# Kernel tuning notes

Hardware: AMD Instinct MI355X
Metric: run time of the kernel (lower is better)

## Reference

```python
import jax, jax.numpy as jnp
import numpy as np
from jax import lax

K = 47          # SH coefficient count
HID = 96        # cascade hidden channels
S = 300         # sampling directions
NC = 4          # number of cascades
IDX = np.r_[0:16, 45:47]  # low-order SH indices used by c_init


def _conv(x, w, bias):
    # x: (B, C, D, H, W); w: (O, I, kd, kh, kw)
    y = lax.conv_general_dilated(x, w, (1, 1, 1), 'VALID',
                                 dimension_numbers=('NCDHW', 'OIDHW', 'NCDHW'))
    return y + bias[None, :, None, None, None]


def _cascade(c, w1, b1, w2, b2, w3, b3):
    # c: (B, D, H, W, 47, 1) -> (B, D-2, H-2, W-2, 94, 1)
    x = jnp.transpose(c[..., 0], (0, 4, 1, 2, 3))       # (B,47,D,H,W)
    x = jax.nn.relu(_conv(x, w1, b1))                    # valid 3x3x3 -> spatial-2
    x = jax.nn.relu(_conv(x, w2, b2))                    # 1x1x1
    x = _conv(x, w3, b3)                                 # 1x1x1 -> 94 channels
    return jnp.transpose(x, (0, 2, 3, 4, 1))[..., None]


def _bsolve(A, rhs):
    # A: (B,K,K) identical across voxels; rhs: (B,D,H,W,K,1)
    # Factor once per batch, apply to all voxel RHS vectors at once.
    B, D, H, W, Kk, _ = rhs.shape
    r = rhs[..., 0].reshape(B, D * H * W, Kk).swapaxes(1, 2)  # (B,K,N)
    x = jnp.linalg.solve(A, r)
    return x.swapaxes(1, 2).reshape(B, D, H, W, Kk, 1)


def _gate(cc):
    return cc[..., :K, :] * jax.nn.sigmoid(cc[..., K:, :])


def setup_inputs() -> dict:
    key = jax.random.key(0)
    ks = jax.random.split(key, 8)
    B, D, H, W = 1, 48, 48, 48
    sc = 0.05
    inp = {
        'b': jax.random.normal(ks[0], (B, D, H, W, S, 1), jnp.float32),
        'AQ': jax.random.normal(ks[1], (B, S, K), jnp.float32) * 0.1,
        'w1': jax.random.normal(ks[2], (NC, HID, K, 3, 3, 3), jnp.float32) * sc,
        'b1': jnp.zeros((NC, HID), jnp.float32),
        'w2': jax.random.normal(ks[3], (NC, HID, HID, 1, 1, 1), jnp.float32) * sc,
        'b2': jnp.zeros((NC, HID), jnp.float32),
        'w3': jax.random.normal(ks[4], (NC, 2 * K, HID, 1, 1, 1), jnp.float32) * sc,
        'b3': jnp.zeros((NC, 2 * K), jnp.float32),
        'deep_reg': jnp.float32(0.05),
    }
    return inp


def reference(b, AQ, w1, b1, w2, b2, w3, b3, deep_reg):
    # AQ^T b per voxel: (B,D,H,W,47,1); AQ^T AQ once per batch: (B,47,47)
    AQ_Tb = jnp.einsum('bnk,bdhwn->bdhwk', AQ, b[..., 0])[..., None]
    AQ_TAQ = jnp.einsum('bnk,bnl->bkl', AQ, AQ)

    # --- c_init: low-order (18-coef) regularized least squares ---
    AQs = AQ[:, :, IDX]                                   # (B,300,18)
    A18 = jnp.einsum('bnk,bnl->bkl', AQs, AQs) + 0.01 * jnp.eye(18, dtype=AQ.dtype)
    c_hat = _bsolve(A18, AQ_Tb[..., IDX, :])
    c = jnp.zeros(b.shape[:4] + (K, 1), b.dtype)
    c = c.at[..., :16, :].set(c_hat[..., :16, :])
    c = c.at[..., 45:, :].set(c_hat[..., 16:, :])

    # --- cascades + data consistency ---
    A = AQ_TAQ + deep_reg * jnp.eye(K, dtype=AQ.dtype)
    for i in range(NC):
        cc = _cascade(c, w1[i], b1[i], w2[i], b2[i], w3[i], b3[i])
        if i == 0:
            g = _gate(cc)
        else:
            g = c[:, 1:-1, 1:-1, 1:-1] + _gate(cc)       # residual connection
        n = i + 1
        c = _bsolve(A, AQ_Tb[:, n:-n, n:-n, n:-n] + deep_reg * g)
    return c
```

## Files before the change

kernel.cpp:

```cpp
#include <hip/hip_runtime.h>
#include <math.h>

#define NS 300
#define NK 47
#define NHID 96
#define NFULL 48

typedef __attribute__((ext_vector_type(8))) short bf16x8;
typedef __attribute__((ext_vector_type(4))) float f32x4;
typedef __attribute__((ext_vector_type(4))) short s16x4;

__device__ __forceinline__ float sigmoidf(float x){ return 1.0f/(1.0f+expf(-x)); }
__device__ __forceinline__ short f2bf(float f){
    union { float f; unsigned u; } v; v.f = f;
    unsigned r = v.u + 0x7fffu + ((v.u >> 16) & 1u);
    return (short)(r >> 16);
}
__device__ __forceinline__ float bf2f(short s){
    union { unsigned u; float f; } v; v.u = ((unsigned)(unsigned short)s) << 16;
    return v.f;
}
__device__ __forceinline__ unsigned pk(short lo, short hi){
    return (unsigned)(unsigned short)lo | ((unsigned)(unsigned short)hi << 16);
}


#define AQP 328
#define P47 72
#define P18 40
__global__ __launch_bounds__(256) void prep_small(const float* __restrict__ AQ,
                           const float* __restrict__ dreg_p,
                           float* __restrict__ Ainv18, short* __restrict__ Ainvbf,
                           short* __restrict__ Bseq){
    __shared__ __align__(16) char smem[93824];
    short* AQh = (short*)smem;
    short* AQl = AQh + 48*AQP;
    float* Gf  = (float*)(smem + 62976);
    short* M47 = (short*)smem;
    short* M18 = (short*)(smem + 72960);
    float* rs47 = (float*)(smem + 93440);
    float* rs18 = rs47 + 48;
    float* shc  = rs18 + 32;

    const int tid = threadIdx.x;
    const int lane = tid & 63;
    const int wv  = tid >> 6;
    const int l15 = lane & 15;
    const int lhi = lane >> 4;
    const float dreg = dreg_p[0];

    #pragma unroll 4
    for (int idx = tid; idx < 48*AQP; idx += 256){
        int k = idx / AQP, n = idx - k*AQP;
        float a = (k < 47 && n < 300) ? AQ[n*NK + k] : 0.f;
        short h = f2bf(a);
        short l = f2bf(a - bf2f(h));
        AQh[idx] = h; AQl[idx] = l;
        if (n < 320){
            int step = n >> 5, lh = (n >> 3) & 3, j = n & 7;
            int t = k >> 4, kl = k & 15;
            int base = ((step*3 + t)*2)*512 + (lh*16 + kl)*8 + j;
            Bseq[base]       = h;
            Bseq[base + 512] = l;
        }
    }
    __syncthreads();

    const int t0 = wv, t1 = wv + 4, t2 = wv + 8;
    f32x4 g0, g1, g2;
    {
        auto gram = [&](int t) -> f32x4 {
            int tt = (t < 9) ? t : t - 9;
            int k0 = (tt/3)*16, l0 = (tt%3)*16;
            f32x4 a = (f32x4){0.f,0.f,0.f,0.f};
            for (int ks = 0; ks < 10; ++ks){
                int off = ks*32 + lhi*8;
                bf16x8 ph = *(const bf16x8*)&AQh[(k0+l15)*AQP + off];
                bf16x8 pl = *(const bf16x8*)&AQl[(k0+l15)*AQP + off];
                bf16x8 qh = *(const bf16x8*)&AQh[(l0+l15)*AQP + off];
                bf16x8 ql = *(const bf16x8*)&AQl[(l0+l15)*AQP + off];
                a = __builtin_amdgcn_mfma_f32_16x16x32_bf16(ph, qh, a, 0,0,0);
                a = __builtin_amdgcn_mfma_f32_16x16x32_bf16(pl, qh, a, 0,0,0);
                a = __builtin_amdgcn_mfma_f32_16x16x32_bf16(ph, ql, a, 0,0,0);
            }
            return a;
        };
        g0 = gram(t0); g1 = gram(t1); g2 = gram(t2);
    }
    __syncthreads();

    for (int i = tid; i < 8*48*P47; i += 256) M47[i] = 0;
    for (int i = tid; i < 8*32*P18; i += 256) M18[i] = 0;
    {
        auto wrG = [&](int t, f32x4 a){
            if (t < 9){
                int k0 = (t/3)*16, l0 = (t%3)*16;
                #pragma unroll
                for (int r = 0; r < 4; ++r)
                    Gf[(k0 + lhi*4 + r)*52 + (l0 + l15)] = a[r];
            }
        };
        wrG(t0,g0); wrG(t1,g1); wrG(t2,g2);
    }
    __syncthreads();

    short* Ah  = M47;            short* Al  = M47 + 3456;
    short* Xah = M47 + 2*3456;   short* Xal = M47 + 3*3456;
    short* Xbh = M47 + 4*3456;   short* Xbl = M47 + 5*3456;
    short* Zh  = M47 + 6*3456;   short* Zl  = M47 + 7*3456;
    short* Bh8 = M18;            short* Bl8 = M18 + 1280;
    short* Xah8= M18 + 2*1280;   short* Xal8= M18 + 3*1280;
    short* Xbh8= M18 + 4*1280;   short* Xbl8= M18 + 5*1280;
    short* Zh8 = M18 + 6*1280;   short* Zl8 = M18 + 7*1280;

    {
        auto wrA = [&](int t, f32x4 a){
            if (t < 9){
                int k0 = (t/3)*16, l0 = (t%3)*16;
                #pragma unroll
                for (int r = 0; r < 4; ++r){
                    int k = k0 + lhi*4 + r, l = l0 + l15;
                    float v = (k < 47 && l < 47) ? a[r] + (k==l ? dreg : 0.f)
                                                 : ((k==l) ? 1.f : 0.f);
                    short h = f2bf(v);
                    Ah[k*P47 + l] = h;
                    Al[k*P47 + l] = f2bf(v - bf2f(h));
                }
            }
        };
        wrA(t0,g0); wrA(t1,g1); wrA(t2,g2);
    }
    if (tid < 48){
        float s = 1.f;
        if (tid < 47){
            s = dreg;
            for (int l = 0; l < 47; ++l) s += fabsf(Gf[tid*52 + l]);
        }
        rs47[tid] = s;
    }
    if (tid >= 64 && tid < 96){
        int r = tid - 64;
        float s = 1.f;
        if (r < 18){
            int gk = (r < 16) ? r : r + 29;
            s = 0.f;
            for (int l = 0; l < 18; ++l){
                int gl = (l < 16) ? l : l + 29;
                s += fabsf(Gf[gk*52 + gl] + ((l==r) ? 0.01f : 0.f));
            }
        }
        rs18[r] = s;
    }
    for (int e = tid; e < 32*32; e += 256){
        int k = e >> 5, l = e & 31;
        float v;
        if (k < 18 && l < 18){
            int gk = (k < 16) ? k : k + 29;
            int gl = (l < 16) ? l : l + 29;
            v = Gf[gk*52 + gl] + ((k==l) ? 0.01f : 0.f);
        } else v = (k==l) ? 1.f : 0.f;
        short h = f2bf(v);
        Bh8[k*P18 + l] = h;
        Bl8[k*P18 + l] = f2bf(v - bf2f(h));
    }
    __syncthreads();

    if (tid == 0){
        float m = 0.f;
        for (int i = 0; i < 48; ++i) m = fmaxf(m, rs47[i]);
        shc[0] = 1.f / m;
    }
    if (tid == 1){
        float m = 0.f;
        for (int i = 0; i < 32; ++i) m = fmaxf(m, rs18[i]);
        shc[1] = 1.f / m;
    }
    __syncthreads();

    if (tid < 48){
        float c = shc[0];
        short h = f2bf(c);
        Xah[tid*P47 + tid] = h;
        Xal[tid*P47 + tid] = f2bf(c - bf2f(h));
    } else if (tid >= 64 && tid < 96){
        int r = tid - 64;
        float c = shc[1];
        short h = f2bf(c);
        Xah8[r*P18 + r] = h;
        Xal8[r*P18 + r] = f2bf(c - bf2f(h));
    }
    __syncthreads();

    auto mmT = [&](int t, const short* Ph, const short* Pl,
                   const short* Qh, const short* Ql) -> f32x4 {
        int tt = (t < 9) ? t : t - 9;
        int k0 = (tt/3)*16, l0 = (tt%3)*16;
        f32x4 a = (f32x4){0.f,0.f,0.f,0.f};
        #pragma unroll
        for (int kk = 0; kk < 2; ++kk){
            int off = kk*32 + lhi*8;
            bf16x8 ph = *(const bf16x8*)&Ph[(k0+l15)*P47 + off];
            bf16x8 pl = *(const bf16x8*)&Pl[(k0+l15)*P47 + off];
            bf16x8 qh = *(const bf16x8*)&Qh[(l0+l15)*P47 + off];
            bf16x8 ql = *(const bf16x8*)&Ql[(l0+l15)*P47 + off];
            a = __builtin_amdgcn_mfma_f32_16x16x32_bf16(ph, qh, a, 0,0,0);
            a = __builtin_amdgcn_mfma_f32_16x16x32_bf16(pl, qh, a, 0,0,0);
            a = __builtin_amdgcn_mfma_f32_16x16x32_bf16(ph, ql, a, 0,0,0);
        }
        return a;
    };
    auto mm8 = [&](const short* Ph, const short* Pl,
                   const short* Qh, const short* Ql) -> f32x4 {
        int k0 = (wv >> 1)*16, l0 = (wv & 1)*16;
        int off = lhi*8;
        bf16x8 ph = *(const bf16x8*)&Ph[(k0+l15)*P18 + off];
        bf16x8 pl = *(const bf16x8*)&Pl[(k0+l15)*P18 + off];
        bf16x8 qh = *(const bf16x8*)&Qh[(l0+l15)*P18 + off];
        bf16x8 ql = *(const bf16x8*)&Ql[(l0+l15)*P18 + off];
        f32x4 a = (f32x4){0.f,0.f,0.f,0.f};
        a = __builtin_amdgcn_mfma_f32_16x16x32_bf16(ph, qh, a, 0,0,0);
        a = __builtin_amdgcn_mfma_f32_16x16x32_bf16(pl, qh, a, 0,0,0);
        a = __builtin_amdgcn_mfma_f32_16x16x32_bf16(ph, ql, a, 0,0,0);
        return a;
    };

    short *Xch = Xah, *Xcl = Xal, *Xnh = Xbh, *Xnl = Xbl;
    short *Xch8 = Xah8, *Xcl8 = Xal8, *Xnh8 = Xbh8, *Xnl8 = Xbl8;

    for (int it = 0; it < 10; ++it){
        f32x4 y0 = mmT(t0, Ah, Al, Xch, Xcl);
        f32x4 y1 = mmT(t1, Ah, Al, Xch, Xcl);
        f32x4 y2 = mmT(t2, Ah, Al, Xch, Xcl);
        f32x4 y8 = mm8(Bh8, Bl8, Xch8, Xcl8);
        auto wrZ = [&](int t, f32x4 a){
            if (t < 9){
                int k0 = (t/3)*16, l0 = (t%3)*16;
                #pragma unroll
                for (int r = 0; r < 4; ++r){
                    int k = k0 + lhi*4 + r, l = l0 + l15;
                    float z = ((k==l) ? 2.f : 0.f) - a[r];
                    short h = f2bf(z);
                    Zh[k*P47 + l] = h;
                    Zl[k*P47 + l] = f2bf(z - bf2f(h));
                }
            }
        };
        wrZ(t0,y0); wrZ(t1,y1); wrZ(t2,y2);
        {
            int k0 = (wv >> 1)*16, l0 = (wv & 1)*16;
            #pragma unroll
            for (int r = 0; r < 4; ++r){
                int k = k0 + lhi*4 + r, l = l0 + l15;
                float z = ((k==l) ? 2.f : 0.f) - y8[r];
                short h = f2bf(z);
                Zh8[k*P18 + l] = h;
                Zl8[k*P18 + l] = f2bf(z - bf2f(h));
            }
        }
        __syncthreads();
        f32x4 x0 = mmT(t0, Xch, Xcl, Zh, Zl);
        f32x4 x1 = mmT(t1, Xch, Xcl, Zh, Zl);
        f32x4 x2 = mmT(t2, Xch, Xcl, Zh, Zl);
        f32x4 x8 = mm8(Xch8, Xcl8, Zh8, Zl8);
        if (it < 9){
            auto wrX = [&](int t, f32x4 a){
                if (t < 9){
                    int k0 = (t/3)*16, l0 = (t%3)*16;
                    #pragma unroll
                    for (int r = 0; r < 4; ++r){
                        int k = k0 + lhi*4 + r, l = l0 + l15;
                        short h = f2bf(a[r]);
                        Xnh[k*P47 + l] = h;
                        Xnl[k*P47 + l] = f2bf(a[r] - bf2f(h));
                    }
                }
            };
            wrX(t0,x0); wrX(t1,x1); wrX(t2,x2);
            int k0 = (wv >> 1)*16, l0 = (wv & 1)*16;
            #pragma unroll
            for (int r = 0; r < 4; ++r){
                int k = k0 + lhi*4 + r, l = l0 + l15;
                short h = f2bf(x8[r]);
                Xnh8[k*P18 + l] = h;
                Xnl8[k*P18 + l] = f2bf(x8[r] - bf2f(h));
            }
        } else {
            auto wrF = [&](int t, f32x4 a){
                if (t < 9){
                    int k0 = (t/3)*16, l0 = (t%3)*16;
                    #pragma unroll
                    for (int r = 0; r < 4; ++r){
                        int k = k0 + lhi*4 + r, l = l0 + l15;
                        float v = (k < 47 && l < 47) ? a[r] : 0.f;
                        Ainvbf[k*64 + l] = f2bf(v);
                    }
                }
            };
            wrF(t0,x0); wrF(t1,x1); wrF(t2,x2);
            int k0 = (wv >> 1)*16, l0 = (wv & 1)*16;
            #pragma unroll
            for (int r = 0; r < 4; ++r){
                int k = k0 + lhi*4 + r, l = l0 + l15;
                if (k < 18 && l < 18) Ainv18[k*18 + l] = x8[r];
            }
        }
        __syncthreads();
        short* tp;
        tp = Xch; Xch = Xnh; Xnh = tp;
        tp = Xcl; Xcl = Xnl; Xnl = tp;
        tp = Xch8; Xch8 = Xnh8; Xnh8 = tp;
        tp = Xcl8; Xcl8 = Xnl8; Xnl8 = tp;
    }

    for (int e = tid; e < 48*16; e += 256){
        int k = e >> 4, j = e & 15;
        Ainvbf[k*64 + 48 + j] = 0;
    }
}

__global__ __launch_bounds__(256) void aqtb_mfma(const float* __restrict__ b,
                                                 const short* __restrict__ Bseq,
                                                 float* __restrict__ AQ_Tb){
    const int lane = threadIdx.x & 63;
    const int wv   = threadIdx.x >> 6;
    const int l15  = lane & 15;
    const int lhi  = lane >> 4;
    const int vrow = blockIdx.x*64 + wv*16 + l15;
    const float* brow = b + (size_t)vrow*NS;
    const short* bs = Bseq + lane*8;

    f32x4 acc[3];
    #pragma unroll
    for (int t = 0; t < 3; ++t) acc[t] = (f32x4){0.f,0.f,0.f,0.f};

    f32x4 q[3][2];
    #pragma unroll
    for (int s = 0; s < 3; ++s){
        const int n0 = s*32 + lhi*8;
        q[s][0] = *(const f32x4*)(brow + n0);
        q[s][1] = *(const f32x4*)(brow + n0 + 4);
    }

    #pragma unroll
    for (int step = 0; step < 10; ++step){
        float x[8];
        #pragma unroll
        for (int j = 0; j < 4; ++j){
            x[j]     = q[step%3][0][j];
            x[4 + j] = q[step%3][1][j];
        }
        if (step + 3 < 9){
            const int n0 = (step+3)*32 + lhi*8;
            q[step%3][0] = *(const f32x4*)(brow + n0);
            q[step%3][1] = *(const f32x4*)(brow + n0 + 4);
        } else if (step + 3 == 9){
            const int n0 = 288 + lhi*8;
            #pragma unroll
            for (int j = 0; j < 4; ++j){
                int n = n0 + j;
                q[step%3][0][j] = (n < NS) ? brow[n] : 0.f;
                int n2 = n0 + 4 + j;
                q[step%3][1][j] = (n2 < NS) ? brow[n2] : 0.f;
            }
        }
        bf16x8 Ah, Al;
        #pragma unroll
        for (int j = 0; j < 8; ++j){
            short h = f2bf(x[j]);
            Ah[j] = h;
            Al[j] = f2bf(x[j] - bf2f(h));
        }
        const short* bstep = bs + step*3072;
        #pragma unroll
        for (int t = 0; t < 3; ++t){
            bf16x8 Bh = *(const bf16x8*)(bstep + t*1024);
            bf16x8 Bl = *(const bf16x8*)(bstep + t*1024 + 512);
            acc[t] = __builtin_amdgcn_mfma_f32_16x16x32_bf16(Ah, Bh, acc[t], 0, 0, 0);
            acc[t] = __builtin_amdgcn_mfma_f32_16x16x32_bf16(Al, Bh, acc[t], 0, 0, 0);
            acc[t] = __builtin_amdgcn_mfma_f32_16x16x32_bf16(Ah, Bl, acc[t], 0, 0, 0);
        }
    }

    const int vbase = blockIdx.x*64 + wv*16 + lhi*4;
    #pragma unroll
    for (int t = 0; t < 3; ++t){
        int k = t*16 + l15;
        if (k < NK){
            #pragma unroll
            for (int r = 0; r < 4; ++r)
                AQ_Tb[(size_t)(vbase + r)*48 + k] = acc[t][r];
        }
    }
}

__global__ void conv_w1_bf16(const float* __restrict__ w1, short* __restrict__ wbf){
    int idx = blockIdx.x*256 + threadIdx.x;
    if (idx >= 4*27*96) return;
    int o = idx % 96; int rest = idx / 96; int s = rest % 27; int i = rest / 27;
    const float* src = w1 + ((size_t)i*96 + o)*1269 + s;
    short* dst = wbf + (size_t)idx*64;
    #pragma unroll
    for (int ci = 0; ci < 47; ++ci) dst[ci] = f2bf(src[ci*27]);
    #pragma unroll
    for (int ci = 47; ci < 64; ++ci) dst[ci] = 0;
}

__global__ void conv_w23_bf16(const float* __restrict__ w2, const float* __restrict__ w3,
                              short* __restrict__ w2bf, short* __restrict__ w3bf){
    int idx = blockIdx.x*256 + threadIdx.x;
    if (idx >= 768) return;
    if (idx < 384){
        const float* src = w2 + (size_t)idx*96;
        short* dst = w2bf + (size_t)idx*96;
        for (int k = 0; k < 96; ++k) dst[k] = f2bf(src[k]);
    } else {
        int j = idx - 384;
        int i = j / 96, o = j % 96;
        short* dst = w3bf + (size_t)j*96;
        if (o < 94){
            const float* src = w3 + ((size_t)i*94 + o)*96;
            for (int k = 0; k < 96; ++k) dst[k] = f2bf(src[k]);
        } else {
            for (int k = 0; k < 96; ++k) dst[k] = 0;
        }
    }
}

__global__ void init_c(const float* __restrict__ AQ_Tb, const float* __restrict__ Ainv18,
                       short* __restrict__ c64, int nvox){
    int v = blockIdx.x*blockDim.x + threadIdx.x;
    if (v >= nvox) return;
    float rhs[18];
    {
        const float* row = AQ_Tb + (size_t)v*48;
        f32x4 r0 = *(const f32x4*)(row + 0);
        f32x4 r1 = *(const f32x4*)(row + 4);
        f32x4 r2 = *(const f32x4*)(row + 8);
        f32x4 r3 = *(const f32x4*)(row + 12);
        #pragma unroll
        for (int j = 0; j < 4; ++j){
            rhs[j] = r0[j]; rhs[4+j] = r1[j]; rhs[8+j] = r2[j]; rhs[12+j] = r3[j];
        }
        rhs[16] = row[45];
        rhs[17] = row[46];
    }
    short row[64];
    #pragma unroll
    for (int k = 0; k < 64; ++k) row[k] = 0;
    #pragma unroll
    for (int r = 0; r < 18; ++r){
        float acc = 0.f;
        #pragma unroll
        for (int j = 0; j < 18; ++j) acc += Ainv18[r*18 + j] * rhs[j];
        row[(r < 16) ? r : 29 + r] = f2bf(acc);
    }
    int x = v % 48; int t2 = v / 48; int y = t2 % 48; int z = t2 / 48;
    short* base = c64 + (size_t)(z*48 + y)*3072;
    #pragma unroll
    for (int g = 0; g < 8; ++g)
        *(bf16x8*)(base + (size_t)(g*48 + x)*8) = *(const bf16x8*)&row[g*8];
}

__device__ __forceinline__ void stage_w(const short* __restrict__ src, short* dst, int tid){
    #pragma unroll
    for (int it = 0; it < 5; ++it){
        int d = (it*512 + tid) * 16;
        if (d < 36864){
            bf16x8 v = *(const bf16x8*)((const char*)src + d);
            int ds = d ^ (((d >> 7) & 7) << 4);
            *(bf16x8*)((char*)dst + ds) = v;
        }
    }
}

__global__ __launch_bounds__(512, 4) void conv1_mfma(const short* __restrict__ c64,
                                                     const short* __restrict__ wbf,
                                                     const float* __restrict__ b1,
                                                     short* __restrict__ h,
                                                     int Ni, int Mi){
    __shared__ short wlds[2][18432];
    const int tid = threadIdx.x;
    const int lane = tid & 63;
    const int wid  = tid >> 6;
    const int l15 = lane & 15;
    const int lhi = lane >> 4;
    const int z0 = blockIdx.z;
    const int x0 = blockIdx.x * 16;
    const int yw = blockIdx.y * 16 + wid * 2;

    f32x4 acc[2][6];
    #pragma unroll
    for (int yr = 0; yr < 2; ++yr)
        #pragma unroll
        for (int t = 0; t < 6; ++t) acc[yr][t] = (f32x4){0.f,0.f,0.f,0.f};

    stage_w(wbf, &wlds[0][0], tid);

    const int grpstride = Ni*8;
    for (int p = 0; p < 9; ++p){
        __syncthreads();
        if (p < 8) stage_w(wbf + (size_t)(p+1)*18432, &wlds[(p+1)&1][0], tid);
        const char* wb = (const char*)&wlds[p&1][0];
        const int dz = p / 3;
        const int dy = p - dz*3;
        const int gzN = (z0 + dz)*Ni;

        #pragma unroll
        for (int dx = 0; dx < 3; ++dx){
            int gx = min(x0 + l15 + dx, Ni-1);
            const short* arow[2];
            #pragma unroll
            for (int yr = 0; yr < 2; ++yr){
                int gy = min(yw + yr + dy, Ni-1);
                arow[yr] = c64 + (size_t)(gzN + gy)*Ni*64 + (size_t)lhi*grpstride + gx*8;
            }
            #pragma unroll
            for (int kk = 0; kk < 2; ++kk){
                bf16x8 a0 = *(const bf16x8*)(arow[0] + kk*4*grpstride);
                bf16x8 a1 = *(const bf16x8*)(arow[1] + kk*4*grpstride);
                #pragma unroll
                for (int t = 0; t < 6; ++t){
                    int d = ((dx*96 + t*16 + l15)*64 + kk*32 + lhi*8) * 2;
                    d ^= ((d >> 7) & 7) << 4;
                    bf16x8 b = *(const bf16x8*)(wb + d);
                    acc[0][t] = __builtin_amdgcn_mfma_f32_16x16x32_bf16(a0, b, acc[0][t], 0, 0, 0);
                    acc[1][t] = __builtin_amdgcn_mfma_f32_16x16x32_bf16(a1, b, acc[1][t], 0, 0, 0);
                }
            }
        }
    }

    #pragma unroll
    for (int yr = 0; yr < 2; ++yr){
        int yy = yw + yr;
        if (yy >= Mi) continue;
        #pragma unroll
        for (int t = 0; t < 6; ++t){
            int och = t*16 + l15;
            float bias = b1[och];
            #pragma unroll
            for (int r = 0; r < 4; ++r){
                int xx = x0 + lhi*4 + r;
                if (xx < Mi){
                    size_t vo = ((size_t)(z0*Mi + yy)*Mi + xx)*NHID + och;
                    h[vo] = f2bf(fmaxf(acc[yr][t][r] + bias, 0.f));
                }
            }
        }
    }
}

__global__ __launch_bounds__(256) void cascade_mfma(const short* __restrict__ h,
                                                    const short* __restrict__ cin64,
                                                    const float* __restrict__ AQ_Tb,
                                                    const short* __restrict__ w2bf,
                                                    const float* __restrict__ b2,
                                                    const short* __restrict__ w3bf,
                                                    const float* __restrict__ b3,
                                                    const short* __restrict__ Ainvbf,
                                                    const float* __restrict__ dreg_p,
                                                    short* __restrict__ c64out,
                                                    float* __restrict__ fout,
                                                    int Mi, int off, int iter, int final_i){
    __shared__ short bufA[64][112];
    __shared__ short bufB[64][112];
    const int tid = threadIdx.x;
    const int lane = tid & 63;
    const int wv  = tid >> 6;
    const int l15 = lane & 15;
    const int lhi = lane >> 4;
    const int nvox = Mi*Mi*Mi;
    const int v0 = blockIdx.x * 64;
    const float dreg = dreg_p[0];

    for (int f = tid; f < 64*24; f += 256){
        int v = f / 24, c = f % 24;
        int gv = v0 + v;
        s16x4 val = (s16x4){0,0,0,0};
        if (gv < nvox) val = *(const s16x4*)(h + (size_t)gv*NHID + c*4);
        *(s16x4*)&bufA[v][c*4] = val;
    }
    __syncthreads();

    const int vox = wv*16 + l15;

    {
        f32x4 acc2[6];
        #pragma unroll
        for (int m = 0; m < 6; ++m) acc2[m] = (f32x4){0.f,0.f,0.f,0.f};
        #pragma unroll
        for (int ks = 0; ks < 3; ++ks){
            bf16x8 bfr = *(const bf16x8*)&bufA[vox][lhi*8 + ks*32];
            #pragma unroll
            for (int m = 0; m < 6; ++m){
                bf16x8 a = *(const bf16x8*)(w2bf + (size_t)(m*16 + l15)*96 + lhi*8 + ks*32);
                acc2[m] = __builtin_amdgcn_mfma_f32_16x16x32_bf16(a, bfr, acc2[m], 0, 0, 0);
            }
        }
        #pragma unroll
        for (int m = 0; m < 6; ++m){
            int o0 = m*16 + lhi*4;
            float x0 = fmaxf(acc2[m][0] + b2[o0+0], 0.f);
            float x1 = fmaxf(acc2[m][1] + b2[o0+1], 0.f);
            float x2 = fmaxf(acc2[m][2] + b2[o0+2], 0.f);
            float x3 = fmaxf(acc2[m][3] + b2[o0+3], 0.f);
            *(unsigned*)&bufB[vox][o0]     = pk(f2bf(x0), f2bf(x1));
            *(unsigned*)&bufB[vox][o0 + 2] = pk(f2bf(x2), f2bf(x3));
        }
    }

    {
        f32x4 acc3[6];
        #pragma unroll
        for (int m = 0; m < 6; ++m) acc3[m] = (f32x4){0.f,0.f,0.f,0.f};
        #pragma unroll
        for (int ks = 0; ks < 3; ++ks){
            bf16x8 bfr = *(const bf16x8*)&bufB[vox][lhi*8 + ks*32];
            #pragma unroll
            for (int m = 0; m < 6; ++m){
                bf16x8 a = *(const bf16x8*)(w3bf + (size_t)(m*16 + l15)*96 + lhi*8 + ks*32);
                acc3[m] = __builtin_amdgcn_mfma_f32_16x16x32_bf16(a, bfr, acc3[m], 0, 0, 0);
            }
        }
        #pragma unroll
        for (int m = 0; m < 6; ++m){
            int o0 = m*16 + lhi*4;
            float xv[4];
            #pragma unroll
            for (int e = 0; e < 4; ++e){
                int o = o0 + e;
                xv[e] = (o < 94) ? acc3[m][e] + b3[o] : 0.f;
            }
            if (o0 + 3 < 47){
                *(unsigned*)&bufA[vox][o0]     = pk(f2bf(xv[0]), f2bf(xv[1]));
                *(unsigned*)&bufA[vox][o0 + 2] = pk(f2bf(xv[2]), f2bf(xv[3]));
            } else {
                #pragma unroll
                for (int e = 0; e < 4; ++e){
                    int o = o0 + e;
                    bufA[vox][o + (o >= 47)] = f2bf(xv[e]);
                }
            }
        }
    }
    __syncthreads();

    short (*rhsL)[64] = (short(*)[64])&bufB[0][0];
    {
        int v = tid >> 2, q = tid & 3;
        int gv = v0 + v;
        int z = 0, y = 0, x = 0;
        bool live = (gv < nvox);
        if (live){
            z = gv / (Mi*Mi);
            int r = gv % (Mi*Mi);
            y = r / Mi; x = r % Mi;
        }
        const int Nin = Mi + 2;
        const size_t rbase = (size_t)((z+1)*Nin + (y+1))*Nin*64;
        const float* aqr = AQ_Tb + ((size_t)((z+off)*NFULL + (y+off))*NFULL + (x+off))*48;

        auto do_group = [&](int g){
            const int k0 = g*8;
            bf16x8 cc1 = *(const bf16x8*)&bufA[v][k0];
            bf16x8 cc2 = *(const bf16x8*)&bufA[v][48 + k0];
            bf16x8 cv = (bf16x8){0,0,0,0,0,0,0,0};
            if (iter > 0)
                cv = *(const bf16x8*)&cin64[rbase + (size_t)(g*Nin + (x+1))*8];
            f32x4 aq0 = *(const f32x4*)(aqr + k0);
            f32x4 aq1 = *(const f32x4*)(aqr + k0 + 4);
            short outs[8];
            #pragma unroll
            for (int j = 0; j < 8; ++j){
                int k = k0 + j;
                if (live && k < 47){
                    float gt = bf2f(cc1[j]) * sigmoidf(bf2f(cc2[j]));
                    if (iter > 0) gt += bf2f(cv[j]);
                    float aq = (j < 4) ? aq0[j] : aq1[j-4];
                    outs[j] = f2bf(aq + dreg * gt);
                } else outs[j] = 0;
            }
            *(bf16x8*)&rhsL[v][k0] = *(const bf16x8*)outs;
        };
        do_group(q);
        if (q < 2){
            do_group(q + 4);
        } else {
            *(bf16x8*)&rhsL[v][48 + (q - 2)*8] = (bf16x8){0,0,0,0,0,0,0,0};
        }
    }
    __syncthreads();

    {
        f32x4 accS[3];
        #pragma unroll
        for (int m = 0; m < 3; ++m) accS[m] = (f32x4){0.f,0.f,0.f,0.f};
        #pragma unroll
        for (int ks = 0; ks < 2; ++ks){
            bf16x8 bfr = *(const bf16x8*)&rhsL[vox][lhi*8 + ks*32];
            #pragma unroll
            for (int m = 0; m < 3; ++m){
                bf16x8 a = *(const bf16x8*)(Ainvbf + (size_t)(m*16 + l15)*64 + lhi*8 + ks*32);
                accS[m] = __builtin_amdgcn_mfma_f32_16x16x32_bf16(a, bfr, accS[m], 0, 0, 0);
            }
        }
        int gv = v0 + vox;
        if (gv < nvox){
            if (final_i){
                #pragma unroll
                for (int m = 0; m < 3; ++m){
                    int k0 = m*16 + lhi*4;
                    #pragma unroll
                    for (int r = 0; r < 4; ++r){
                        int k = k0 + r;
                        if (k < 47) fout[(size_t)gv*NK + k] = accS[m][r];
                    }
                }
            } else {
                int z = gv / (Mi*Mi);
                int rr = gv % (Mi*Mi);
                int y = rr / Mi, x = rr % Mi;
                short* base = c64out + (size_t)(z*Mi + y)*Mi*64;
                #pragma unroll
                for (int m = 0; m < 3; ++m){
                    int k0 = m*16 + lhi*4;
                    int g = k0 >> 3, j = k0 & 7;
                    short s0 = f2bf(accS[m][0]);
                    short s1 = f2bf(accS[m][1]);
                    short s2 = f2bf(accS[m][2]);
                    short s3 = (k0 + 3 < 47) ? f2bf(accS[m][3]) : (short)0;
                    short* ad = base + (size_t)(g*Mi + x)*8 + j;
                    *(unsigned*)(ad)     = pk(s0, s1);
                    *(unsigned*)(ad + 2) = pk(s2, s3);
                }
            }
        }
    }

    if (!final_i){
        for (int f = tid; f < 64*8; f += 256){
            int v = f >> 3, gv = v0 + v;
            if (gv < nvox){
                int u = f & 7;
                int c = 48 + u*2;
                int g = c >> 3, j = c & 7;
                int z = gv / (Mi*Mi);
                int rr = gv % (Mi*Mi);
                int y = rr / Mi, x = rr % Mi;
                *(unsigned*)&c64out[(size_t)(z*Mi + y)*Mi*64 + (size_t)(g*Mi + x)*8 + j] = 0;
            }
        }
    }
}

extern "C" void kernel_launch(void* const* d_in, const int* in_sizes, int n_in,
                              void* d_out, int out_size, void* d_ws, size_t ws_size,
                              hipStream_t stream){
    const float* b    = (const float*)d_in[0];
    const float* AQ   = (const float*)d_in[1];
    const float* w1   = (const float*)d_in[2];
    const float* b1   = (const float*)d_in[3];
    const float* w2   = (const float*)d_in[4];
    const float* b2   = (const float*)d_in[5];
    const float* w3   = (const float*)d_in[6];
    const float* b3   = (const float*)d_in[7];
    const float* dreg = (const float*)d_in[8];
    float* out = (float*)d_out;
    float* ws  = (float*)d_ws;

    const size_t NV48 = (size_t)48*48*48;
    float* Ainv18 = ws;
    float* AQ_Tb  = ws + 336;
    short* hbuf   = (short*)(AQ_Tb + NV48*48);
    short* w1bf   = hbuf + (size_t)46*46*46*NHID;
    short* w2bf   = w1bf + (size_t)4*27*96*64;
    short* w3bf   = w2bf + (size_t)4*96*96;
    short* Ainvbf = w3bf + (size_t)4*96*96;
    short* Bseq   = Ainvbf + 48*64;
    short* c64A   = Bseq + 30720;
    short* c64B   = c64A + NV48*64 + 32768;

    prep_small<<<1, 256, 0, stream>>>(AQ, dreg, Ainv18, Ainvbf, Bseq);
    conv_w1_bf16<<<(4*27*96 + 255)/256, 256, 0, stream>>>(w1, w1bf);
    conv_w23_bf16<<<3, 256, 0, stream>>>(w2, w3, w2bf, w3bf);
    aqtb_mfma<<<(int)(NV48/64), 256, 0, stream>>>(b, Bseq, AQ_Tb);
    init_c<<<(int)((NV48 + 255)/256), 256, 0, stream>>>(AQ_Tb, Ainv18, c64A, (int)NV48);

    short* ccur = c64A;
    short* cnext = c64B;
    for (int i = 0; i < 4; ++i){
        int Ni = 48 - 2*i;
        int Mi = Ni - 2;
        dim3 g1((Mi + 15)/16, (Mi + 15)/16, Mi);
        conv1_mfma<<<g1, 512, 0, stream>>>(ccur, w1bf + (size_t)i*27*96*64, b1 + i*96,
                                           hbuf, Ni, Mi);
        int nv = Mi*Mi*Mi;
        int fin = (i == 3) ? 1 : 0;
        cascade_mfma<<<(nv + 63)/64, 256, 0, stream>>>(
            hbuf, ccur, AQ_Tb, w2bf + (size_t)i*9216, b2 + i*96,
            w3bf + (size_t)i*9216, b3 + i*94, Ainvbf, dreg, cnext, out, Mi, i+1, i, fin);
        short* t = ccur; ccur = cnext; cnext = t;
    }
}
```

Before: 420.1 us.

## Fuse 3x3x3 conv1 with 1x1 cascade layers and data-consistency solve

Merges the conv1 kernel and the cascade kernel into one. The conv1 output tile is now written to shared memory and consumed in place by the 1x1x1 layers, the gating and the Ainv multiply, processed in two passes of 128 voxels. This removes the global hidden-activation buffer and its write and re-read each cascade, plus one launch per iteration. In exchange, shared memory per block grows and the 1x1 stages run at conv1's block shape, including padded edge voxels.

```diff
diff --git a/kernel.cpp b/kernel.cpp
--- a/kernel.cpp
+++ b/kernel.cpp
@@ -473,12 +473,23 @@
     }
 }
 
-__global__ __launch_bounds__(512, 4) void conv1_mfma(const short* __restrict__ c64,
-                                                     const short* __restrict__ wbf,
-                                                     const float* __restrict__ b1,
-                                                     short* __restrict__ h,
-                                                     int Ni, int Mi){
-    __shared__ short wlds[2][18432];
+__global__ __launch_bounds__(512, 4) void conv1_cascade(
+        const short* __restrict__ c64,
+        const short* __restrict__ wbf,
+        const float* __restrict__ b1,
+        const float* __restrict__ AQ_Tb,
+        const short* __restrict__ w2bf, const float* __restrict__ b2,
+        const short* __restrict__ w3bf, const float* __restrict__ b3,
+        const short* __restrict__ Ainvbf,
+        const float* __restrict__ dreg_p,
+        short* __restrict__ c64out,
+        float* __restrict__ fout,
+        int Ni, int Mi, int off, int iter, int final_i){
+    __shared__ __align__(16) char smem[79872];
+    short (*hl)[104]   = (short(*)[104])smem;
+    short (*bufB)[104] = (short(*)[104])(smem + 53248);
+    short (*rhsL)[64]  = (short(*)[64])(smem + 53248);
+
     const int tid = threadIdx.x;
     const int lane = tid & 63;
     const int wid  = tid >> 6;
@@ -486,7 +497,9 @@
     const int lhi = lane >> 4;
     const int z0 = blockIdx.z;
     const int x0 = blockIdx.x * 16;
-    const int yw = blockIdx.y * 16 + wid * 2;
+    const int y0 = blockIdx.y * 16;
+    const int yw = y0 + wid * 2;
+    const float dreg = dreg_p[0];
 
     f32x4 acc[2][6];
     #pragma unroll
@@ -494,13 +507,13 @@
         #pragma unroll
         for (int t = 0; t < 6; ++t) acc[yr][t] = (f32x4){0.f,0.f,0.f,0.f};
 
-    stage_w(wbf, &wlds[0][0], tid);
+    stage_w(wbf, (short*)smem, tid);
 
     const int grpstride = Ni*8;
     for (int p = 0; p < 9; ++p){
         __syncthreads();
-        if (p < 8) stage_w(wbf + (size_t)(p+1)*18432, &wlds[(p+1)&1][0], tid);
-        const char* wb = (const char*)&wlds[p&1][0];
+        if (p < 8) stage_w(wbf + (size_t)(p+1)*18432, (short*)(smem + (size_t)((p+1)&1)*36864), tid);
+        const char* wb = (const char*)(smem + (size_t)(p&1)*36864);
         const int dz = p / 3;
         const int dy = p - dz*3;
         const int gzN = (z0 + dz)*Ni;
@@ -530,224 +543,188 @@
         }
     }
 
+    __syncthreads();
     #pragma unroll
     for (int yr = 0; yr < 2; ++yr){
-        int yy = yw + yr;
-        if (yy >= Mi) continue;
+        int rowb = (wid*2 + yr)*16;
         #pragma unroll
         for (int t = 0; t < 6; ++t){
             int och = t*16 + l15;
             float bias = b1[och];
             #pragma unroll
             for (int r = 0; r < 4; ++r){
-                int xx = x0 + lhi*4 + r;
-                if (xx < Mi){
-                    size_t vo = ((size_t)(z0*Mi + yy)*Mi + xx)*NHID + och;
-                    h[vo] = f2bf(fmaxf(acc[yr][t][r] + bias, 0.f));
-                }
-            }
-        }
-    }
-}
-
-__global__ __launch_bounds__(256) void cascade_mfma(const short* __restrict__ h,
-                                                    const short* __restrict__ cin64,
-                                                    const float* __restrict__ AQ_Tb,
-                                                    const short* __restrict__ w2bf,
-                                                    const float* __restrict__ b2,
-                                                    const short* __restrict__ w3bf,
-                                                    const float* __restrict__ b3,
-                                                    const short* __restrict__ Ainvbf,
-                                                    const float* __restrict__ dreg_p,
-                                                    short* __restrict__ c64out,
-                                                    float* __restrict__ fout,
-                                                    int Mi, int off, int iter, int final_i){
-    __shared__ short bufA[64][112];
-    __shared__ short bufB[64][112];
-    const int tid = threadIdx.x;
-    const int lane = tid & 63;
-    const int wv  = tid >> 6;
-    const int l15 = lane & 15;
-    const int lhi = lane >> 4;
-    const int nvox = Mi*Mi*Mi;
-    const int v0 = blockIdx.x * 64;
-    const float dreg = dreg_p[0];
-
-    for (int f = tid; f < 64*24; f += 256){
-        int v = f / 24, c = f % 24;
-        int gv = v0 + v;
-        s16x4 val = (s16x4){0,0,0,0};
-        if (gv < nvox) val = *(const s16x4*)(h + (size_t)gv*NHID + c*4);
-        *(s16x4*)&bufA[v][c*4] = val;
+                hl[rowb + lhi*4 + r][och] = f2bf(fmaxf(acc[yr][t][r] + bias, 0.f));
+            }
+        }
     }
     __syncthreads();
 
-    const int vox = wv*16 + l15;
-
-    {
-        f32x4 acc2[6];
-        #pragma unroll
-        for (int m = 0; m < 6; ++m) acc2[m] = (f32x4){0.f,0.f,0.f,0.f};
-        #pragma unroll
-        for (int ks = 0; ks < 3; ++ks){
-            bf16x8 bfr = *(const bf16x8*)&bufA[vox][lhi*8 + ks*32];
+    const int Nin = Ni;
+    for (int pass = 0; pass < 2; ++pass){
+        if (pass) __syncthreads();
+        const int vox  = wid*16 + l15;
+        const int vloc = pass*128 + vox;
+
+        {
+            f32x4 acc2[6];
+            #pragma unroll
+            for (int m = 0; m < 6; ++m) acc2[m] = (f32x4){0.f,0.f,0.f,0.f};
+            #pragma unroll
+            for (int ks = 0; ks < 3; ++ks){
+                bf16x8 bfr = *(const bf16x8*)&hl[vloc][lhi*8 + ks*32];
+                #pragma unroll
+                for (int m = 0; m < 6; ++m){
+                    bf16x8 a = *(const bf16x8*)(w2bf + (size_t)(m*16 + l15)*96 + lhi*8 + ks*32);
+                    acc2[m] = __builtin_amdgcn_mfma_f32_16x16x32_bf16(a, bfr, acc2[m], 0, 0, 0);
+                }
+            }
             #pragma unroll
             for (int m = 0; m < 6; ++m){
-                bf16x8 a = *(const bf16x8*)(w2bf + (size_t)(m*16 + l15)*96 + lhi*8 + ks*32);
-                acc2[m] = __builtin_amdgcn_mfma_f32_16x16x32_bf16(a, bfr, acc2[m], 0, 0, 0);
-            }
-        }
-        #pragma unroll
-        for (int m = 0; m < 6; ++m){
-            int o0 = m*16 + lhi*4;
-            float x0 = fmaxf(acc2[m][0] + b2[o0+0], 0.f);
-            float x1 = fmaxf(acc2[m][1] + b2[o0+1], 0.f);
-            float x2 = fmaxf(acc2[m][2] + b2[o0+2], 0.f);
-            float x3 = fmaxf(acc2[m][3] + b2[o0+3], 0.f);
-            *(unsigned*)&bufB[vox][o0]     = pk(f2bf(x0), f2bf(x1));
-            *(unsigned*)&bufB[vox][o0 + 2] = pk(f2bf(x2), f2bf(x3));
-        }
-    }
-
-    {
-        f32x4 acc3[6];
-        #pragma unroll
-        for (int m = 0; m < 6; ++m) acc3[m] = (f32x4){0.f,0.f,0.f,0.f};
-        #pragma unroll
-        for (int ks = 0; ks < 3; ++ks){
-            bf16x8 bfr = *(const bf16x8*)&bufB[vox][lhi*8 + ks*32];
+                int o0 = m*16 + lhi*4;
+                float x0v = fmaxf(acc2[m][0] + b2[o0+0], 0.f);
+                float x1v = fmaxf(acc2[m][1] + b2[o0+1], 0.f);
+                float x2v = fmaxf(acc2[m][2] + b2[o0+2], 0.f);
+                float x3v = fmaxf(acc2[m][3] + b2[o0+3], 0.f);
+                *(unsigned*)&bufB[vox][o0]     = pk(f2bf(x0v), f2bf(x1v));
+                *(unsigned*)&bufB[vox][o0 + 2] = pk(f2bf(x2v), f2bf(x3v));
+            }
+        }
+
+        {
+            f32x4 acc3[6];
+            #pragma unroll
+            for (int m = 0; m < 6; ++m) acc3[m] = (f32x4){0.f,0.f,0.f,0.f};
+            #pragma unroll
+            for (int ks = 0; ks < 3; ++ks){
+                bf16x8 bfr = *(const bf16x8*)&bufB[vox][lhi*8 + ks*32];
+                #pragma unroll
+                for (int m = 0; m < 6; ++m){
+                    bf16x8 a = *(const bf16x8*)(w3bf + (size_t)(m*16 + l15)*96 + lhi*8 + ks*32);
+                    acc3[m] = __builtin_amdgcn_mfma_f32_16x16x32_bf16(a, bfr, acc3[m], 0, 0, 0);
+                }
+            }
             #pragma unroll
             for (int m = 0; m < 6; ++m){
-                bf16x8 a = *(const bf16x8*)(w3bf + (size_t)(m*16 + l15)*96 + lhi*8 + ks*32);
-                acc3[m] = __builtin_amdgcn_mfma_f32_16x16x32_bf16(a, bfr, acc3[m], 0, 0, 0);
-            }
-        }
-        #pragma unroll
-        for (int m = 0; m < 6; ++m){
-            int o0 = m*16 + lhi*4;
-            float xv[4];
-            #pragma unroll
-            for (int e = 0; e < 4; ++e){
-                int o = o0 + e;
-                xv[e] = (o < 94) ? acc3[m][e] + b3[o] : 0.f;
-            }
-            if (o0 + 3 < 47){
-                *(unsigned*)&bufA[vox][o0]     = pk(f2bf(xv[0]), f2bf(xv[1]));
-                *(unsigned*)&bufA[vox][o0 + 2] = pk(f2bf(xv[2]), f2bf(xv[3]));
-            } else {
+                int o0 = m*16 + lhi*4;
+                float xv[4];
                 #pragma unroll
                 for (int e = 0; e < 4; ++e){
                     int o = o0 + e;
-                    bufA[vox][o + (o >= 47)] = f2bf(xv[e]);
-                }
-            }
-        }
-    }
-    __syncthreads();
-
-    short (*rhsL)[64] = (short(*)[64])&bufB[0][0];
-    {
-        int v = tid >> 2, q = tid & 3;
-        int gv = v0 + v;
-        int z = 0, y = 0, x = 0;
-        bool live = (gv < nvox);
-        if (live){
-            z = gv / (Mi*Mi);
-            int r = gv % (Mi*Mi);
-            y = r / Mi; x = r % Mi;
-        }
-        const int Nin = Mi + 2;
-        const size_t rbase = (size_t)((z+1)*Nin + (y+1))*Nin*64;
-        const float* aqr = AQ_Tb + ((size_t)((z+off)*NFULL + (y+off))*NFULL + (x+off))*48;
-
-        auto do_group = [&](int g){
-            const int k0 = g*8;
-            bf16x8 cc1 = *(const bf16x8*)&bufA[v][k0];
-            bf16x8 cc2 = *(const bf16x8*)&bufA[v][48 + k0];
-            bf16x8 cv = (bf16x8){0,0,0,0,0,0,0,0};
-            if (iter > 0)
-                cv = *(const bf16x8*)&cin64[rbase + (size_t)(g*Nin + (x+1))*8];
-            f32x4 aq0 = *(const f32x4*)(aqr + k0);
-            f32x4 aq1 = *(const f32x4*)(aqr + k0 + 4);
-            short outs[8];
-            #pragma unroll
-            for (int j = 0; j < 8; ++j){
-                int k = k0 + j;
-                if (live && k < 47){
-                    float gt = bf2f(cc1[j]) * sigmoidf(bf2f(cc2[j]));
-                    if (iter > 0) gt += bf2f(cv[j]);
-                    float aq = (j < 4) ? aq0[j] : aq1[j-4];
-                    outs[j] = f2bf(aq + dreg * gt);
-                } else outs[j] = 0;
-            }
-            *(bf16x8*)&rhsL[v][k0] = *(const bf16x8*)outs;
-        };
-        do_group(q);
-        if (q < 2){
-            do_group(q + 4);
-        } else {
-            *(bf16x8*)&rhsL[v][48 + (q - 2)*8] = (bf16x8){0,0,0,0,0,0,0,0};
-        }
-    }
-    __syncthreads();
-
-    {
-        f32x4 accS[3];
-        #pragma unroll
-        for (int m = 0; m < 3; ++m) accS[m] = (f32x4){0.f,0.f,0.f,0.f};
-        #pragma unroll
-        for (int ks = 0; ks < 2; ++ks){
-            bf16x8 bfr = *(const bf16x8*)&rhsL[vox][lhi*8 + ks*32];
-            #pragma unroll
-            for (int m = 0; m < 3; ++m){
-                bf16x8 a = *(const bf16x8*)(Ainvbf + (size_t)(m*16 + l15)*64 + lhi*8 + ks*32);
-                accS[m] = __builtin_amdgcn_mfma_f32_16x16x32_bf16(a, bfr, accS[m], 0, 0, 0);
-            }
-        }
-        int gv = v0 + vox;
-        if (gv < nvox){
-            if (final_i){
+                    xv[e] = (o < 94) ? acc3[m][e] + b3[o] : 0.f;
+                }
+                if (o0 + 3 < 47){
+                    *(unsigned*)&hl[vloc][o0]     = pk(f2bf(xv[0]), f2bf(xv[1]));
+                    *(unsigned*)&hl[vloc][o0 + 2] = pk(f2bf(xv[2]), f2bf(xv[3]));
+                } else {
+                    #pragma unroll
+                    for (int e = 0; e < 4; ++e){
+                        int o = o0 + e;
+                        hl[vloc][o + (o >= 47)] = f2bf(xv[e]);
+                    }
+                }
+            }
+        }
+        __syncthreads();
+
+        {
+            int row = tid >> 2, q = tid & 3;
+            int v = pass*128 + row;
+            int yl = v >> 4, xl = v & 15;
+            int y = y0 + yl, x = x0 + xl;
+            bool live = (x < Mi) && (y < Mi);
+            int yc = live ? y : 0, xc = live ? x : 0;
+            const size_t rbase = (size_t)((z0+1)*Nin + (yc+1))*Nin*64;
+            const float* aqr = AQ_Tb + ((size_t)((z0+off)*NFULL + (yc+off))*NFULL + (xc+off))*48;
+
+            auto do_group = [&](int g){
+                const int k0 = g*8;
+                bf16x8 cc1 = *(const bf16x8*)&hl[v][k0];
+                bf16x8 cc2 = *(const bf16x8*)&hl[v][48 + k0];
+                bf16x8 cv = (bf16x8){0,0,0,0,0,0,0,0};
+                if (iter > 0)
+                    cv = *(const bf16x8*)&c64[rbase + (size_t)(g*Nin + (xc+1))*8];
+                f32x4 aq0 = *(const f32x4*)(aqr + k0);
+                f32x4 aq1 = *(const f32x4*)(aqr + k0 + 4);
+                short outs[8];
+                #pragma unroll
+                for (int j = 0; j < 8; ++j){
+                    int k = k0 + j;
+                    if (live && k < 47){
+                        float gt = bf2f(cc1[j]) * sigmoidf(bf2f(cc2[j]));
+                        if (iter > 0) gt += bf2f(cv[j]);
+                        float aq = (j < 4) ? aq0[j] : aq1[j-4];
+                        outs[j] = f2bf(aq + dreg * gt);
+                    } else outs[j] = 0;
+                }
+                *(bf16x8*)&rhsL[row][k0] = *(const bf16x8*)outs;
+            };
+            do_group(q);
+            if (q < 2){
+                do_group(q + 4);
+            } else {
+                *(bf16x8*)&rhsL[row][48 + (q - 2)*8] = (bf16x8){0,0,0,0,0,0,0,0};
+            }
+        }
+        __syncthreads();
+
+        {
+            f32x4 accS[3];
+            #pragma unroll
+            for (int m = 0; m < 3; ++m) accS[m] = (f32x4){0.f,0.f,0.f,0.f};
+            #pragma unroll
+            for (int ks = 0; ks < 2; ++ks){
+                bf16x8 bfr = *(const bf16x8*)&rhsL[vox][lhi*8 + ks*32];
                 #pragma unroll
                 for (int m = 0; m < 3; ++m){
-                    int k0 = m*16 + lhi*4;
+                    bf16x8 a = *(const bf16x8*)(Ainvbf + (size_t)(m*16 + l15)*64 + lhi*8 + ks*32);
+                    accS[m] = __builtin_amdgcn_mfma_f32_16x16x32_bf16(a, bfr, accS[m], 0, 0, 0);
+                }
+            }
+            int v = pass*128 + vox;
+            int yl = v >> 4, xl = v & 15;
+            int y = y0 + yl, x = x0 + xl;
+            if (x < Mi && y < Mi){
+                if (final_i){
+                    int gv = (z0*Mi + y)*Mi + x;
                     #pragma unroll
-                    for (int r = 0; r < 4; ++r){
-                        int k = k0 + r;
-                        if (k < 47) fout[(size_t)gv*NK + k] = accS[m][r];
+                    for (int m = 0; m < 3; ++m){
+                        int k0 = m*16 + lhi*4;
+                        #pragma unroll
+                        for (int r = 0; r < 4; ++r){
+                            int k = k0 + r;
+                            if (k < 47) fout[(size_t)gv*NK + k] = accS[m][r];
+                        }
                     }
-                }
-            } else {
-                int z = gv / (Mi*Mi);
-                int rr = gv % (Mi*Mi);
-                int y = rr / Mi, x = rr % Mi;
-                short* base = c64out + (size_t)(z*Mi + y)*Mi*64;
-                #pragma unroll
-                for (int m = 0; m < 3; ++m){
-                    int k0 = m*16 + lhi*4;
-                    int g = k0 >> 3, j = k0 & 7;
-                    short s0 = f2bf(accS[m][0]);
-                    short s1 = f2bf(accS[m][1]);
-                    short s2 = f2bf(accS[m][2]);
-                    short s3 = (k0 + 3 < 47) ? f2bf(accS[m][3]) : (short)0;
-                    short* ad = base + (size_t)(g*Mi + x)*8 + j;
-                    *(unsigned*)(ad)     = pk(s0, s1);
-                    *(unsigned*)(ad + 2) = pk(s2, s3);
-                }
-            }
-        }
-    }
-
-    if (!final_i){
-        for (int f = tid; f < 64*8; f += 256){
-            int v = f >> 3, gv = v0 + v;
-            if (gv < nvox){
-                int u = f & 7;
-                int c = 48 + u*2;
-                int g = c >> 3, j = c & 7;
-                int z = gv / (Mi*Mi);
-                int rr = gv % (Mi*Mi);
-                int y = rr / Mi, x = rr % Mi;
-                *(unsigned*)&c64out[(size_t)(z*Mi + y)*Mi*64 + (size_t)(g*Mi + x)*8 + j] = 0;
+                } else {
+                    short* base = c64out + (size_t)(z0*Mi + y)*Mi*64;
+                    #pragma unroll
+                    for (int m = 0; m < 3; ++m){
+                        int k0 = m*16 + lhi*4;
+                        int g = k0 >> 3, j = k0 & 7;
+                        short s0 = f2bf(accS[m][0]);
+                        short s1 = f2bf(accS[m][1]);
+                        short s2 = f2bf(accS[m][2]);
+                        short s3 = (k0 + 3 < 47) ? f2bf(accS[m][3]) : (short)0;
+                        short* ad = base + (size_t)(g*Mi + x)*8 + j;
+                        *(unsigned*)(ad)     = pk(s0, s1);
+                        *(unsigned*)(ad + 2) = pk(s2, s3);
+                    }
+                }
+            }
+        }
+
+        if (!final_i){
+            for (int f = tid; f < 128*8; f += 512){
+                int vl = f >> 3;
+                int v = pass*128 + vl;
+                int yl = v >> 4, xl = v & 15;
+                int y = y0 + yl, x = x0 + xl;
+                if (x < Mi && y < Mi){
+                    int u = f & 7;
+                    int c = 48 + u*2;
+                    int g = c >> 3, j = c & 7;
+                    *(unsigned*)&c64out[(size_t)(z0*Mi + y)*Mi*64 + (size_t)(g*Mi + x)*8 + j] = 0;
+                }
             }
         }
     }
@@ -771,8 +748,7 @@
     const size_t NV48 = (size_t)48*48*48;
     float* Ainv18 = ws;
     float* AQ_Tb  = ws + 336;
-    short* hbuf   = (short*)(AQ_Tb + NV48*48);
-    short* w1bf   = hbuf + (size_t)46*46*46*NHID;
+    short* w1bf   = (short*)(AQ_Tb + NV48*48);
     short* w2bf   = w1bf + (size_t)4*27*96*64;
     short* w3bf   = w2bf + (size_t)4*96*96;
     short* Ainvbf = w3bf + (size_t)4*96*96;
@@ -792,13 +768,11 @@
         int Ni = 48 - 2*i;
         int Mi = Ni - 2;
         dim3 g1((Mi + 15)/16, (Mi + 15)/16, Mi);
-        conv1_mfma<<<g1, 512, 0, stream>>>(ccur, w1bf + (size_t)i*27*96*64, b1 + i*96,
-                                           hbuf, Ni, Mi);
-        int nv = Mi*Mi*Mi;
         int fin = (i == 3) ? 1 : 0;
-        cascade_mfma<<<(nv + 63)/64, 256, 0, stream>>>(
-            hbuf, ccur, AQ_Tb, w2bf + (size_t)i*9216, b2 + i*96,
-            w3bf + (size_t)i*9216, b3 + i*94, Ainvbf, dreg, cnext, out, Mi, i+1, i, fin);
+        conv1_cascade<<<g1, 512, 0, stream>>>(
+            ccur, w1bf + (size_t)i*27*96*64, b1 + i*96, AQ_Tb,
+            w2bf + (size_t)i*9216, b2 + i*96, w3bf + (size_t)i*9216, b3 + i*94,
+            Ainvbf, dreg, cnext, out, Ni, Mi, i+1, i, fin);
         short* t = ccur; ccur = cnext; cnext = t;
     }
 }
```

After: 722.1 us. +71.9%, slower.
